# Kernel optimization log

Hardware: AMD Instinct MI355X
Metric: run time of the kernel (lower is better)

## Reference

```python
import jax, jax.numpy as jnp
import numpy as np

HIDDEN = 1024
N_HEADS = 16
HEAD_DIM = HIDDEN // N_HEADS  # 64
SCALE = HEAD_DIM ** -0.5
B, QL, KVL = 2, 2048, 4096


def setup_inputs() -> dict:
    key = jax.random.key(0)
    ks = jax.random.split(key, 7)
    s = 0.02
    return {
        "query_states": jax.random.normal(ks[0], (B, QL, HIDDEN), jnp.float32),
        "key_states": jax.random.normal(ks[1], (B, KVL, HIDDEN), jnp.float32),
        "value_states": jax.random.normal(ks[2], (B, KVL, HIDDEN), jnp.float32),
        # torch nn.Linear weights: shape [out, in], applied as x @ W.T
        "Wq": jax.random.normal(ks[3], (HIDDEN, HIDDEN), jnp.float32) * s,
        "Wk": jax.random.normal(ks[4], (HIDDEN, HIDDEN), jnp.float32) * s,
        "Wv": jax.random.normal(ks[5], (HIDDEN, HIDDEN), jnp.float32) * s,
        "Wo": jax.random.normal(ks[6], (HIDDEN, HIDDEN), jnp.float32) * s,
    }


def reference(query_states, key_states, value_states, Wq, Wk, Wv, Wo):
    b, ql, _ = query_states.shape
    kvl = key_states.shape[1]
    # projections (torch Linear: x @ W.T)
    q = query_states @ Wq.T  # [b, ql, H]
    k = key_states @ Wk.T    # [b, kvl, H]
    v = value_states @ Wv.T  # [b, kvl, H]
    # split heads -> [b, h, s, d]
    q = q.reshape(b, ql, N_HEADS, HEAD_DIM).transpose(0, 2, 1, 3)
    k = k.reshape(b, kvl, N_HEADS, HEAD_DIM).transpose(0, 2, 1, 3)
    v = v.reshape(b, kvl, N_HEADS, HEAD_DIM).transpose(0, 2, 1, 3)
    # scores [b, h, ql, kvl]
    scores = jnp.einsum("bhqd,bhkd->bhqk", q, k) * SCALE
    attn = jax.nn.softmax(scores, axis=-1)
    out = jnp.einsum("bhqk,bhkd->bhqd", attn, v)  # [b, h, ql, d]
    out = out.transpose(0, 2, 1, 3).reshape(b, ql, HIDDEN)
    return out @ Wo.T
```

## Files before the change

kernel.cpp:

```cpp
#include <hip/hip_runtime.h>

#define HID   1024
#define NH    16
#define HD    64
#define QL    2048
#define KVL   4096
#define NB    2
#define QSCALE 0.180336880111120426f

typedef short s8v  __attribute__((ext_vector_type(8)));
typedef short s4v  __attribute__((ext_vector_type(4)));
typedef float f4v  __attribute__((ext_vector_type(4)));

__device__ __forceinline__ unsigned short f2bf(float f) {
  unsigned int u = __builtin_bit_cast(unsigned int, f);
  u += 0x7FFFu + ((u >> 16) & 1u);
  return (unsigned short)(u >> 16);
}

__device__ __forceinline__ float fexp2(float x) {
#if __has_builtin(__builtin_amdgcn_exp2f)
  return __builtin_amdgcn_exp2f(x);
#else
  return exp2f(x);
#endif
}

__global__ __launch_bounds__(256)
void cast_all(const float* __restrict__ q, const float* __restrict__ k,
              const float* __restrict__ v, const float* __restrict__ wq,
              const float* __restrict__ wk, const float* __restrict__ wv,
              const float* __restrict__ wo, unsigned short* __restrict__ dst) {
  size_t c = (size_t)blockIdx.x * 256 + threadIdx.x;
  const float* src; size_t lc; float sc = 1.0f;
  if (c < 524288)       { src = q;  lc = c; }
  else if (c < 1572864) { src = k;  lc = c - 524288; }
  else if (c < 2621440) { src = v;  lc = c - 1572864; }
  else if (c < 2752512) { src = wq; lc = c - 2621440; sc = QSCALE; }
  else if (c < 2883584) { src = wk; lc = c - 2752512; }
  else if (c < 3014656) { src = wv; lc = c - 2883584; }
  else                  { src = wo; lc = c - 3014656; }
  const float4* p = (const float4*)(src + lc * 8);
  float4 a = p[0], b = p[1];
  union { s8v v8; unsigned short h[8]; } u;
  u.h[0] = f2bf(a.x * sc); u.h[1] = f2bf(a.y * sc);
  u.h[2] = f2bf(a.z * sc); u.h[3] = f2bf(a.w * sc);
  u.h[4] = f2bf(b.x * sc); u.h[5] = f2bf(b.y * sc);
  u.h[6] = f2bf(b.z * sc); u.h[7] = f2bf(b.w * sc);
  *(s8v*)(dst + c * 8) = u.v8;
}

typedef const __attribute__((address_space(1))) unsigned int* gas_t;
typedef __attribute__((address_space(3))) unsigned int*       las_t;

__device__ __forceinline__ void gl_lds16(const unsigned short* g, unsigned short* l) {
  __builtin_amdgcn_global_load_lds((gas_t)(const void*)g, (las_t)(void*)l, 16, 0, 0);
}

template <int NJ, bool OUT_BF16>
__device__ __forceinline__ void gemm_body(const unsigned short* __restrict__ A,
                                          const unsigned short* __restrict__ B,
                                          void* __restrict__ Cv, int N, int K,
                                          int bx, int by,
                                          unsigned short* As, unsigned short* Bs) {
  constexpr int TBN = NJ * 32;
  constexpr int WN  = TBN / 2;
  const int tid  = threadIdx.x;
  const int wave = tid >> 6, lane = tid & 63;
  const int wm = wave >> 1, wn = wave & 1;
  const int quad = lane >> 4, l15 = lane & 15;
  const int row0 = by * 128;
  const int col0 = bx * TBN;
  const int srow = lane >> 2;
  const int scol = (lane & 3) * 8;

  f4v acc[4][NJ] = {};

  for (int k0 = 0; k0 < K; k0 += 32) {
    __syncthreads();
#pragma unroll
    for (int cc = 0; cc < 2; cc++) {
      int c = wave + cc * 4;
      gl_lds16(A + (size_t)(row0 + c * 16 + srow) * K + k0 + scol, &As[c * 512]);
    }
    if (NJ == 4) {
#pragma unroll
      for (int cc = 0; cc < 2; cc++) {
        int c = wave + cc * 4;
        gl_lds16(B + (size_t)(col0 + c * 16 + srow) * K + k0 + scol, &Bs[c * 512]);
      }
    } else {
      gl_lds16(B + (size_t)(col0 + wave * 16 + srow) * K + k0 + scol, &Bs[wave * 512]);
    }
    __syncthreads();

    s8v af[4], bf[NJ];
#pragma unroll
    for (int i = 0; i < 4; i++)
      af[i] = *(const s8v*)&As[(wm * 64 + i * 16 + l15) * 32 + quad * 8];
#pragma unroll
    for (int j = 0; j < NJ; j++)
      bf[j] = *(const s8v*)&Bs[(wn * WN + j * 16 + l15) * 32 + quad * 8];
#pragma unroll
    for (int i = 0; i < 4; i++)
#pragma unroll
      for (int j = 0; j < NJ; j++)
        acc[i][j] = __builtin_amdgcn_mfma_f32_16x16x32_bf16(af[i], bf[j],
                                                            acc[i][j], 0, 0, 0);
  }

#pragma unroll
  for (int i = 0; i < 4; i++) {
#pragma unroll
    for (int j = 0; j < NJ; j++) {
      int r = row0 + wm * 64 + i * 16 + quad * 4;
      int c = col0 + wn * WN + j * 16 + l15;
#pragma unroll
      for (int reg = 0; reg < 4; reg++) {
        float v = acc[i][j][reg];
        if constexpr (OUT_BF16)
          ((unsigned short*)Cv)[(size_t)(r + reg) * N + c] = f2bf(v);
        else
          ((float*)Cv)[(size_t)(r + reg) * N + c] = v;
      }
    }
  }
}

__global__ __launch_bounds__(256, 2)
void proj_fused(const unsigned short* __restrict__ qc, const unsigned short* __restrict__ kc,
                const unsigned short* __restrict__ vc, const unsigned short* __restrict__ wqc,
                const unsigned short* __restrict__ wkc, const unsigned short* __restrict__ wvc,
                unsigned short* __restrict__ qp, unsigned short* __restrict__ kp,
                unsigned short* __restrict__ vpt) {
  __shared__ unsigned short As[128 * 32];
  __shared__ unsigned short Bs[128 * 32];
  int bid = blockIdx.x;
  if (bid < 512) {
    gemm_body<2, true>(qc, wqc, qp, HID, HID, bid & 15, bid >> 4, As, Bs);
  } else if (bid < 1536) {
    int l = bid - 512;
    gemm_body<2, true>(kc, wkc, kp, HID, HID, l & 15, l >> 4, As, Bs);
  } else {
    int l = bid - 1536;
    int b = l >> 8, r = l & 255;
    gemm_body<4, true>(wvc, vc + (size_t)b * KVL * HID,
                       vpt + (size_t)b * HID * KVL, KVL, HID, r & 31, r >> 5, As, Bs);
  }
}

__global__ __launch_bounds__(256, 2)
void o_gemm(const unsigned short* __restrict__ ao, const unsigned short* __restrict__ woc,
            float* __restrict__ out) {
  __shared__ unsigned short As[128 * 32];
  __shared__ unsigned short Bs[128 * 32];
  int bid = blockIdx.x;
  gemm_body<2, false>(ao, woc, out, HID, HID, bid & 15, bid >> 4, As, Bs);
}

#define LDSK 40

template <typename T>
__device__ __forceinline__ void stage_tile(unsigned short* dst, const T* src,
                                           int ld, int tid, float sc) {
#pragma unroll
  for (int rep = 0; rep < 2; rep++) {
    int s = rep * 256 + tid;
    int row = s >> 2;
    int cs  = (s & 3) * 8;
    const T* p = src + (size_t)row * ld + cs;
    s8v val;
    if constexpr (sizeof(T) == 4) {
      float4 f0 = *(const float4*)p;
      float4 f1 = *(const float4*)(p + 4);
      union { s8v v; unsigned short h[8]; } u;
      u.h[0] = f2bf(f0.x * sc); u.h[1] = f2bf(f0.y * sc);
      u.h[2] = f2bf(f0.z * sc); u.h[3] = f2bf(f0.w * sc);
      u.h[4] = f2bf(f1.x * sc); u.h[5] = f2bf(f1.y * sc);
      u.h[6] = f2bf(f1.z * sc); u.h[7] = f2bf(f1.w * sc);
      val = u.v;
    } else {
      val = *(const s8v*)p;
    }
    *(s8v*)&dst[row * LDSK + cs] = val;
  }
}

template <typename TA, typename TB, bool OUT_BF16>
__global__ __launch_bounds__(256)
void gemm_conv(const TA* __restrict__ A, const TB* __restrict__ B,
               void* __restrict__ Cv, int M, int N, int K, float bscale,
               long long bz, long long cz) {
  __shared__ unsigned short As[128 * LDSK];
  __shared__ unsigned short Bs[128 * LDSK];
  const TB* Bp = B + (size_t)blockIdx.z * (size_t)bz;
  const int tid  = threadIdx.x;
  const int wave = tid >> 6, lane = tid & 63;
  const int wm = wave >> 1, wn = wave & 1;
  const int quad = lane >> 4, l15 = lane & 15;
  const int row0 = blockIdx.y * 128;
  const int col0 = blockIdx.x * 128;

  f4v acc[4][4] = {};

  for (int k0 = 0; k0 < K; k0 += 32) {
    __syncthreads();
    stage_tile(As, A + (size_t)row0 * K + k0, K, tid, 1.0f);
    stage_tile(Bs, Bp + (size_t)col0 * K + k0, K, tid, bscale);
    __syncthreads();

    s8v af[4], bf[4];
#pragma unroll
    for (int i = 0; i < 4; i++)
      af[i] = *(const s8v*)&As[(wm * 64 + i * 16 + l15) * LDSK + quad * 8];
#pragma unroll
    for (int j = 0; j < 4; j++)
      bf[j] = *(const s8v*)&Bs[(wn * 64 + j * 16 + l15) * LDSK + quad * 8];
#pragma unroll
    for (int i = 0; i < 4; i++)
#pragma unroll
      for (int j = 0; j < 4; j++)
        acc[i][j] = __builtin_amdgcn_mfma_f32_16x16x32_bf16(af[i], bf[j],
                                                            acc[i][j], 0, 0, 0);
  }

  char* Cp = (char*)Cv + (size_t)blockIdx.z * (size_t)cz * (OUT_BF16 ? 2 : 4);
#pragma unroll
  for (int i = 0; i < 4; i++) {
#pragma unroll
    for (int j = 0; j < 4; j++) {
      int r = row0 + wm * 64 + i * 16 + quad * 4;
      int c = col0 + wn * 64 + j * 16 + l15;
#pragma unroll
      for (int reg = 0; reg < 4; reg++) {
        float v = acc[i][j][reg];
        if constexpr (OUT_BF16)
          ((unsigned short*)Cp)[(size_t)(r + reg) * N + c] = f2bf(v);
        else
          ((float*)Cp)[(size_t)(r + reg) * N + c] = v;
      }
    }
  }
}

#define AST 72

__global__ __launch_bounds__(256, 2)
void attn3(const unsigned short* __restrict__ qp,
           const unsigned short* __restrict__ kp,
           const unsigned short* __restrict__ vpt,
           unsigned short* __restrict__ ao) {
  __shared__ unsigned short Ks[64 * AST];
  __shared__ unsigned short Vt[64 * AST];
  __shared__ unsigned short Pt[4][32 * AST];

  const int bid  = blockIdx.x;
  const int qb   = bid & 15;
  const int h    = (bid >> 4) & 15;
  const int b    = bid >> 8;
  const int tid  = threadIdx.x;
  const int wave = tid >> 6, lane = tid & 63;
  const int quad = lane >> 4, l15 = lane & 15;
  const int q0   = qb * 128 + wave * 32;

  int srow[2], scs[2];
#pragma unroll
  for (int rep = 0; rep < 2; rep++) {
    int s = rep * 256 + tid;
    srow[rep] = s >> 3;
    scs[rep]  = (s & 7) * 8;
  }

  s8v qf[2][2];
#pragma unroll
  for (int qt = 0; qt < 2; qt++) {
    const size_t qrow = (size_t)(b * QL + q0 + qt * 16 + l15) * HID + h * HD;
#pragma unroll
    for (int ks = 0; ks < 2; ks++)
      qf[qt][ks] = *(const s8v*)(qp + qrow + ks * 32 + quad * 8);
  }

  float lrun[2] = {0.f, 0.f};
  f4v oacc[2][4] = {};

  const unsigned short* kbase = kp + (size_t)b * KVL * HID + h * HD;
  const unsigned short* vbase = vpt + (size_t)(b * NH + h) * HD * KVL;

  s8v kreg[2], vreg[2];
#pragma unroll
  for (int rep = 0; rep < 2; rep++) {
    kreg[rep] = *(const s8v*)(kbase + (size_t)srow[rep] * HID + scs[rep]);
    vreg[rep] = *(const s8v*)(vbase + (size_t)srow[rep] * KVL + scs[rep]);
  }

  for (int kt = 0; kt < KVL / 64; kt++) {
    __syncthreads();
#pragma unroll
    for (int rep = 0; rep < 2; rep++) {
      *(s8v*)&Ks[srow[rep] * AST + scs[rep]] = kreg[rep];
      *(s8v*)&Vt[srow[rep] * AST + scs[rep]] = vreg[rep];
    }
    if (kt + 1 < KVL / 64) {
      int kv0n = (kt + 1) * 64;
#pragma unroll
      for (int rep = 0; rep < 2; rep++) {
        kreg[rep] = *(const s8v*)(kbase + (size_t)(kv0n + srow[rep]) * HID + scs[rep]);
        vreg[rep] = *(const s8v*)(vbase + (size_t)srow[rep] * KVL + kv0n + scs[rep]);
      }
    }
    __syncthreads();

    f4v sacc[2][4] = {};
#pragma unroll
    for (int nt = 0; nt < 4; nt++) {
      s8v kf0 = *(const s8v*)&Ks[(nt * 16 + l15) * AST + quad * 8];
      s8v kf1 = *(const s8v*)&Ks[(nt * 16 + l15) * AST + 32 + quad * 8];
#pragma unroll
      for (int qt = 0; qt < 2; qt++) {
        sacc[qt][nt] = __builtin_amdgcn_mfma_f32_16x16x32_bf16(kf0, qf[qt][0], sacc[qt][nt], 0, 0, 0);
        sacc[qt][nt] = __builtin_amdgcn_mfma_f32_16x16x32_bf16(kf1, qf[qt][1], sacc[qt][nt], 0, 0, 0);
      }
    }

#pragma unroll
    for (int qt = 0; qt < 2; qt++) {
      float rs = 0.f;
#pragma unroll
      for (int nt = 0; nt < 4; nt++) {
        float p0 = fexp2(sacc[qt][nt][0]);
        float p1 = fexp2(sacc[qt][nt][1]);
        float p2 = fexp2(sacc[qt][nt][2]);
        float p3 = fexp2(sacc[qt][nt][3]);
        rs += (p0 + p1) + (p2 + p3);
        union { s4v v4; unsigned short h[4]; } pk;
        pk.h[0] = f2bf(p0); pk.h[1] = f2bf(p1);
        pk.h[2] = f2bf(p2); pk.h[3] = f2bf(p3);
        *(s4v*)&Pt[wave][(qt * 16 + l15) * AST + nt * 16 + quad * 4] = pk.v4;
      }
      rs += __shfl_xor(rs, 16, 64);
      rs += __shfl_xor(rs, 32, 64);
      lrun[qt] += rs;
    }

#pragma unroll
    for (int ch = 0; ch < 2; ch++) {
      s8v vf[4];
#pragma unroll
      for (int dt = 0; dt < 4; dt++)
        vf[dt] = *(const s8v*)&Vt[(dt * 16 + l15) * AST + ch * 32 + quad * 8];
#pragma unroll
      for (int qt = 0; qt < 2; qt++) {
        s8v pf = *(const s8v*)&Pt[wave][(qt * 16 + l15) * AST + ch * 32 + quad * 8];
#pragma unroll
        for (int dt = 0; dt < 4; dt++)
          oacc[qt][dt] = __builtin_amdgcn_mfma_f32_16x16x32_bf16(pf, vf[dt], oacc[qt][dt], 0, 0, 0);
      }
    }
  }

#pragma unroll
  for (int qt = 0; qt < 2; qt++) {
    float li = 1.0f / lrun[qt];
    float lr[4];
#pragma unroll
    for (int r = 0; r < 4; r++)
      lr[r] = __shfl(li, (lane & 48) + ((lane >> 4) & 3) * 4 + r, 64);
#pragma unroll
    for (int dt = 0; dt < 4; dt++)
#pragma unroll
      for (int r = 0; r < 4; r++) {
        int qq = q0 + qt * 16 + quad * 4 + r;
        int cc = h * HD + dt * 16 + l15;
        ao[(size_t)(b * QL + qq) * HID + cc] = f2bf(oacc[qt][dt][r] * lr[r]);
      }
  }
}

extern "C" void kernel_launch(void* const* d_in, const int* in_sizes, int n_in,
                              void* d_out, int out_size, void* d_ws, size_t ws_size,
                              hipStream_t stream) {
  const float* q  = (const float*)d_in[0];
  const float* k  = (const float*)d_in[1];
  const float* v  = (const float*)d_in[2];
  const float* Wq = (const float*)d_in[3];
  const float* Wk = (const float*)d_in[4];
  const float* Wv = (const float*)d_in[5];
  const float* Wo = (const float*)d_in[6];
  float* out = (float*)d_out;
  char* ws = (char*)d_ws;
  dim3 blk(256);

  const long long MB = 1024 * 1024;
  if (ws_size >= (size_t)88 * MB) {
    unsigned short* qc  = (unsigned short*)(ws);
    unsigned short* kc  = (unsigned short*)(ws + 8 * MB);
    unsigned short* vc  = (unsigned short*)(ws + 24 * MB);
    unsigned short* wqc = (unsigned short*)(ws + 40 * MB);
    unsigned short* wkc = (unsigned short*)(ws + 42 * MB);
    unsigned short* wvc = (unsigned short*)(ws + 44 * MB);
    unsigned short* woc = (unsigned short*)(ws + 46 * MB);
    unsigned short* qp  = (unsigned short*)(ws + 48 * MB);
    unsigned short* kp  = (unsigned short*)(ws + 56 * MB);
    unsigned short* vpt = (unsigned short*)(ws + 72 * MB);
    unsigned short* ao  = (unsigned short*)(ws);

    cast_all<<<12288, blk, 0, stream>>>(q, k, v, Wq, Wk, Wv, Wo, (unsigned short*)ws);
    proj_fused<<<2048, blk, 0, stream>>>(qc, kc, vc, wqc, wkc, wvc, qp, kp, vpt);
    attn3<<<dim3(NB * NH * (QL / 128)), blk, 0, stream>>>(qp, kp, vpt, ao);
    o_gemm<<<512, blk, 0, stream>>>(ao, woc, out);
  } else {
    unsigned short* qp  = (unsigned short*)(ws);
    unsigned short* kp  = (unsigned short*)(ws + 8 * MB);
    unsigned short* vpt = (unsigned short*)(ws + 24 * MB);
    unsigned short* ao  = (unsigned short*)(ws + 40 * MB);

    gemm_conv<float, float, true><<<dim3(8, 32), blk, 0, stream>>>(q, Wq, qp, NB * QL, HID, HID, QSCALE, 0, 0);
    gemm_conv<float, float, true><<<dim3(8, 64), blk, 0, stream>>>(k, Wk, kp, NB * KVL, HID, HID, 1.0f, 0, 0);
    gemm_conv<float, float, true><<<dim3(32, 8, 2), blk, 0, stream>>>(Wv, v, vpt, HID, KVL, HID, 1.0f,
                                                                      (long long)KVL * HID, (long long)HID * KVL);
    attn3<<<dim3(NB * NH * (QL / 128)), blk, 0, stream>>>(qp, kp, vpt, ao);
    gemm_conv<unsigned short, float, false><<<dim3(8, 32), blk, 0, stream>>>(ao, Wo, out, NB * QL, HID, HID, 1.0f, 0, 0);
  }
}
```

Baseline: 320.1 us.

## Enlarge attention query tile and triple-buffer K/V via async LDS loads

Attention blocks now process 256 queries, 64 per wave, and use a three-stage ring of K/V tiles filled with direct global-to-LDS loads and an XOR-swizzled layout instead of register staging with padding. The projection and output GEMMs switch to uniform 128x128 tiles, which halves the block counts. The aim is to raise K/V reuse per load and overlap memory with MFMA work. In exchange, occupancy drops to one block per CU, only 256 attention blocks are launched, and register pressure rises.

```diff
diff --git a/kernel.cpp b/kernel.cpp
--- a/kernel.cpp
+++ b/kernel.cpp
@@ -57,24 +57,22 @@
   __builtin_amdgcn_global_load_lds((gas_t)(const void*)g, (las_t)(void*)l, 16, 0, 0);
 }
 
-template <int NJ, bool OUT_BF16>
+template <bool OUT_BF16>
 __device__ __forceinline__ void gemm_body(const unsigned short* __restrict__ A,
                                           const unsigned short* __restrict__ B,
                                           void* __restrict__ Cv, int N, int K,
                                           int bx, int by,
                                           unsigned short* As, unsigned short* Bs) {
-  constexpr int TBN = NJ * 32;
-  constexpr int WN  = TBN / 2;
   const int tid  = threadIdx.x;
   const int wave = tid >> 6, lane = tid & 63;
   const int wm = wave >> 1, wn = wave & 1;
   const int quad = lane >> 4, l15 = lane & 15;
   const int row0 = by * 128;
-  const int col0 = bx * TBN;
+  const int col0 = bx * 128;
   const int srow = lane >> 2;
   const int scol = (lane & 3) * 8;
 
-  f4v acc[4][NJ] = {};
+  f4v acc[4][4] = {};
 
   for (int k0 = 0; k0 < K; k0 += 32) {
     __syncthreads();
@@ -82,29 +80,21 @@
     for (int cc = 0; cc < 2; cc++) {
       int c = wave + cc * 4;
       gl_lds16(A + (size_t)(row0 + c * 16 + srow) * K + k0 + scol, &As[c * 512]);
-    }
-    if (NJ == 4) {
-#pragma unroll
-      for (int cc = 0; cc < 2; cc++) {
-        int c = wave + cc * 4;
-        gl_lds16(B + (size_t)(col0 + c * 16 + srow) * K + k0 + scol, &Bs[c * 512]);
-      }
-    } else {
-      gl_lds16(B + (size_t)(col0 + wave * 16 + srow) * K + k0 + scol, &Bs[wave * 512]);
+      gl_lds16(B + (size_t)(col0 + c * 16 + srow) * K + k0 + scol, &Bs[c * 512]);
     }
     __syncthreads();
 
-    s8v af[4], bf[NJ];
+    s8v af[4], bf[4];
 #pragma unroll
     for (int i = 0; i < 4; i++)
       af[i] = *(const s8v*)&As[(wm * 64 + i * 16 + l15) * 32 + quad * 8];
 #pragma unroll
-    for (int j = 0; j < NJ; j++)
-      bf[j] = *(const s8v*)&Bs[(wn * WN + j * 16 + l15) * 32 + quad * 8];
+    for (int j = 0; j < 4; j++)
+      bf[j] = *(const s8v*)&Bs[(wn * 64 + j * 16 + l15) * 32 + quad * 8];
 #pragma unroll
     for (int i = 0; i < 4; i++)
 #pragma unroll
-      for (int j = 0; j < NJ; j++)
+      for (int j = 0; j < 4; j++)
         acc[i][j] = __builtin_amdgcn_mfma_f32_16x16x32_bf16(af[i], bf[j],
                                                             acc[i][j], 0, 0, 0);
   }
@@ -112,9 +102,9 @@
 #pragma unroll
   for (int i = 0; i < 4; i++) {
 #pragma unroll
-    for (int j = 0; j < NJ; j++) {
+    for (int j = 0; j < 4; j++) {
       int r = row0 + wm * 64 + i * 16 + quad * 4;
-      int c = col0 + wn * WN + j * 16 + l15;
+      int c = col0 + wn * 64 + j * 16 + l15;
 #pragma unroll
       for (int reg = 0; reg < 4; reg++) {
         float v = acc[i][j][reg];
@@ -136,16 +126,16 @@
   __shared__ unsigned short As[128 * 32];
   __shared__ unsigned short Bs[128 * 32];
   int bid = blockIdx.x;
-  if (bid < 512) {
-    gemm_body<2, true>(qc, wqc, qp, HID, HID, bid & 15, bid >> 4, As, Bs);
-  } else if (bid < 1536) {
-    int l = bid - 512;
-    gemm_body<2, true>(kc, wkc, kp, HID, HID, l & 15, l >> 4, As, Bs);
+  if (bid < 256) {
+    gemm_body<true>(qc, wqc, qp, HID, HID, bid & 7, bid >> 3, As, Bs);
+  } else if (bid < 768) {
+    int l = bid - 256;
+    gemm_body<true>(kc, wkc, kp, HID, HID, l & 7, l >> 3, As, Bs);
   } else {
-    int l = bid - 1536;
+    int l = bid - 768;
     int b = l >> 8, r = l & 255;
-    gemm_body<4, true>(wvc, vc + (size_t)b * KVL * HID,
-                       vpt + (size_t)b * HID * KVL, KVL, HID, r & 31, r >> 5, As, Bs);
+    gemm_body<true>(wvc, vc + (size_t)b * KVL * HID,
+                    vpt + (size_t)b * HID * KVL, KVL, HID, r & 31, r >> 5, As, Bs);
   }
 }
 
@@ -155,7 +145,7 @@
   __shared__ unsigned short As[128 * 32];
   __shared__ unsigned short Bs[128 * 32];
   int bid = blockIdx.x;
-  gemm_body<2, false>(ao, woc, out, HID, HID, bid & 15, bid >> 4, As, Bs);
+  gemm_body<false>(ao, woc, out, HID, HID, bid & 7, bid >> 3, As, Bs);
 }
 
 #define LDSK 40
@@ -245,126 +235,131 @@
 
 #define AST 72
 
-__global__ __launch_bounds__(256, 2)
-void attn3(const unsigned short* __restrict__ qp,
+__global__ __launch_bounds__(256, 1)
+void attn4(const unsigned short* __restrict__ qp,
            const unsigned short* __restrict__ kp,
            const unsigned short* __restrict__ vpt,
            unsigned short* __restrict__ ao) {
-  __shared__ unsigned short Ks[64 * AST];
-  __shared__ unsigned short Vt[64 * AST];
-  __shared__ unsigned short Pt[4][32 * AST];
+  __shared__ unsigned short Ks[3][64 * 64];
+  __shared__ unsigned short Vt[3][64 * 64];
+  __shared__ unsigned short Pt[4][64 * AST];
 
   const int bid  = blockIdx.x;
-  const int qb   = bid & 15;
-  const int h    = (bid >> 4) & 15;
-  const int b    = bid >> 8;
+  const int qb   = bid & 7;
+  const int h    = (bid >> 3) & 15;
+  const int b    = bid >> 7;
   const int tid  = threadIdx.x;
   const int wave = tid >> 6, lane = tid & 63;
   const int quad = lane >> 4, l15 = lane & 15;
-  const int q0   = qb * 128 + wave * 32;
-
-  int srow[2], scs[2];
-#pragma unroll
-  for (int rep = 0; rep < 2; rep++) {
-    int s = rep * 256 + tid;
-    srow[rep] = s >> 3;
-    scs[rep]  = (s & 7) * 8;
-  }
-
-  s8v qf[2][2];
-#pragma unroll
-  for (int qt = 0; qt < 2; qt++) {
-    const size_t qrow = (size_t)(b * QL + q0 + qt * 16 + l15) * HID + h * HD;
-#pragma unroll
-    for (int ks = 0; ks < 2; ks++)
-      qf[qt][ks] = *(const s8v*)(qp + qrow + ks * 32 + quad * 8);
-  }
-
-  float lrun[2] = {0.f, 0.f};
-  f4v oacc[2][4] = {};
+  const int q0   = qb * 256 + wave * 64;
 
   const unsigned short* kbase = kp + (size_t)b * KVL * HID + h * HD;
   const unsigned short* vbase = vpt + (size_t)(b * NH + h) * HD * KVL;
 
-  s8v kreg[2], vreg[2];
-#pragma unroll
-  for (int rep = 0; rep < 2; rep++) {
-    kreg[rep] = *(const s8v*)(kbase + (size_t)srow[rep] * HID + scs[rep]);
-    vreg[rep] = *(const s8v*)(vbase + (size_t)srow[rep] * KVL + scs[rep]);
-  }
-
-  for (int kt = 0; kt < KVL / 64; kt++) {
-    __syncthreads();
-#pragma unroll
-    for (int rep = 0; rep < 2; rep++) {
-      *(s8v*)&Ks[srow[rep] * AST + scs[rep]] = kreg[rep];
-      *(s8v*)&Vt[srow[rep] * AST + scs[rep]] = vreg[rep];
-    }
-    if (kt + 1 < KVL / 64) {
-      int kv0n = (kt + 1) * 64;
-#pragma unroll
-      for (int rep = 0; rep < 2; rep++) {
-        kreg[rep] = *(const s8v*)(kbase + (size_t)(kv0n + srow[rep]) * HID + scs[rep]);
-        vreg[rep] = *(const s8v*)(vbase + (size_t)srow[rep] * KVL + kv0n + scs[rep]);
-      }
-    }
-    __syncthreads();
-
-    f4v sacc[2][4] = {};
+  int prow[2], pcol[2], pbase[2];
+#pragma unroll
+  for (int i = 0; i < 2; i++) {
+    int p = (i * 4 + wave) * 64 + lane;
+    prow[i]  = p >> 3;
+    pcol[i]  = ((p & 7) ^ (prow[i] & 7)) * 8;
+    pbase[i] = (i * 4 + wave) * 512;
+  }
+
+  s8v qf[4][2];
+#pragma unroll
+  for (int nt = 0; nt < 4; nt++) {
+    const size_t qrow = (size_t)(b * QL + q0 + nt * 16 + l15) * HID + h * HD;
+#pragma unroll
+    for (int ks = 0; ks < 2; ks++)
+      qf[nt][ks] = *(const s8v*)(qp + qrow + ks * 32 + quad * 8);
+  }
+
+  float lrun[4] = {0.f, 0.f, 0.f, 0.f};
+  f4v oacc[4][4] = {};
+
+#define STAGE_KV(KT, BI)                                                        \
+  {                                                                             \
+    const unsigned short* kb = kbase + (size_t)((KT) * 64) * HID;               \
+    const unsigned short* vb = vbase + (KT) * 64;                               \
+    _Pragma("unroll")                                                           \
+    for (int i = 0; i < 2; i++) {                                               \
+      gl_lds16(kb + (size_t)prow[i] * HID + pcol[i], &Ks[BI][pbase[i]]);        \
+      gl_lds16(vb + (size_t)prow[i] * KVL + pcol[i], &Vt[BI][pbase[i]]);        \
+    }                                                                           \
+  }
+
+  constexpr int NT = KVL / 64;
+  STAGE_KV(0, 0);
+  STAGE_KV(1, 1);
+  __syncthreads();
+
+  for (int kt = 0; kt < NT; kt++) {
+    const int cur = kt % 3;
+    if (kt + 2 < NT) STAGE_KV(kt + 2, (kt + 2) % 3);
+
+    f4v sacc[4][4] = {};
+#pragma unroll
+    for (int ks = 0; ks < 2; ks++)
+#pragma unroll
+      for (int mt = 0; mt < 4; mt++) {
+        int row = mt * 16 + l15;
+        int xc  = ((ks * 4 + quad) ^ (row & 7)) * 8;
+        s8v kf = *(const s8v*)&Ks[cur][row * 64 + xc];
+#pragma unroll
+        for (int nt = 0; nt < 4; nt++)
+          sacc[mt][nt] = __builtin_amdgcn_mfma_f32_16x16x32_bf16(kf, qf[nt][ks],
+                                                                 sacc[mt][nt], 0, 0, 0);
+      }
+
 #pragma unroll
     for (int nt = 0; nt < 4; nt++) {
-      s8v kf0 = *(const s8v*)&Ks[(nt * 16 + l15) * AST + quad * 8];
-      s8v kf1 = *(const s8v*)&Ks[(nt * 16 + l15) * AST + 32 + quad * 8];
-#pragma unroll
-      for (int qt = 0; qt < 2; qt++) {
-        sacc[qt][nt] = __builtin_amdgcn_mfma_f32_16x16x32_bf16(kf0, qf[qt][0], sacc[qt][nt], 0, 0, 0);
-        sacc[qt][nt] = __builtin_amdgcn_mfma_f32_16x16x32_bf16(kf1, qf[qt][1], sacc[qt][nt], 0, 0, 0);
-      }
-    }
-
-#pragma unroll
-    for (int qt = 0; qt < 2; qt++) {
       float rs = 0.f;
 #pragma unroll
-      for (int nt = 0; nt < 4; nt++) {
-        float p0 = fexp2(sacc[qt][nt][0]);
-        float p1 = fexp2(sacc[qt][nt][1]);
-        float p2 = fexp2(sacc[qt][nt][2]);
-        float p3 = fexp2(sacc[qt][nt][3]);
+      for (int mt = 0; mt < 4; mt++) {
+        float p0 = fexp2(sacc[mt][nt][0]);
+        float p1 = fexp2(sacc[mt][nt][1]);
+        float p2 = fexp2(sacc[mt][nt][2]);
+        float p3 = fexp2(sacc[mt][nt][3]);
         rs += (p0 + p1) + (p2 + p3);
-        union { s4v v4; unsigned short h[4]; } pk;
-        pk.h[0] = f2bf(p0); pk.h[1] = f2bf(p1);
-        pk.h[2] = f2bf(p2); pk.h[3] = f2bf(p3);
-        *(s4v*)&Pt[wave][(qt * 16 + l15) * AST + nt * 16 + quad * 4] = pk.v4;
+        union { s4v v4; unsigned short hh[4]; } pk;
+        pk.hh[0] = f2bf(p0); pk.hh[1] = f2bf(p1);
+        pk.hh[2] = f2bf(p2); pk.hh[3] = f2bf(p3);
+        *(s4v*)&Pt[wave][(nt * 16 + l15) * AST + mt * 16 + quad * 4] = pk.v4;
       }
       rs += __shfl_xor(rs, 16, 64);
       rs += __shfl_xor(rs, 32, 64);
-      lrun[qt] += rs;
+      lrun[nt] += rs;
     }
 
 #pragma unroll
     for (int ch = 0; ch < 2; ch++) {
       s8v vf[4];
 #pragma unroll
-      for (int dt = 0; dt < 4; dt++)
-        vf[dt] = *(const s8v*)&Vt[(dt * 16 + l15) * AST + ch * 32 + quad * 8];
-#pragma unroll
-      for (int qt = 0; qt < 2; qt++) {
+      for (int dt = 0; dt < 4; dt++) {
+        int row = dt * 16 + l15;
+        int xc  = ((ch * 4 + quad) ^ (row & 7)) * 8;
+        vf[dt] = *(const s8v*)&Vt[cur][row * 64 + xc];
+      }
+#pragma unroll
+      for (int qt = 0; qt < 4; qt++) {
         s8v pf = *(const s8v*)&Pt[wave][(qt * 16 + l15) * AST + ch * 32 + quad * 8];
 #pragma unroll
         for (int dt = 0; dt < 4; dt++)
-          oacc[qt][dt] = __builtin_amdgcn_mfma_f32_16x16x32_bf16(pf, vf[dt], oacc[qt][dt], 0, 0, 0);
-      }
-    }
-  }
-
-#pragma unroll
-  for (int qt = 0; qt < 2; qt++) {
+          oacc[qt][dt] = __builtin_amdgcn_mfma_f32_16x16x32_bf16(pf, vf[dt],
+                                                                 oacc[qt][dt], 0, 0, 0);
+      }
+    }
+
+    __syncthreads();
+  }
+
+#pragma unroll
+  for (int qt = 0; qt < 4; qt++) {
     float li = 1.0f / lrun[qt];
     float lr[4];
 #pragma unroll
     for (int r = 0; r < 4; r++)
-      lr[r] = __shfl(li, (lane & 48) + ((lane >> 4) & 3) * 4 + r, 64);
+      lr[r] = __shfl(li, (lane & 48) + quad * 4 + r, 64);
 #pragma unroll
     for (int dt = 0; dt < 4; dt++)
 #pragma unroll
@@ -374,6 +369,7 @@
         ao[(size_t)(b * QL + qq) * HID + cc] = f2bf(oacc[qt][dt][r] * lr[r]);
       }
   }
+#undef STAGE_KV
 }
 
 extern "C" void kernel_launch(void* const* d_in, const int* in_sizes, int n_in,
@@ -405,9 +401,9 @@
     unsigned short* ao  = (unsigned short*)(ws);
 
     cast_all<<<12288, blk, 0, stream>>>(q, k, v, Wq, Wk, Wv, Wo, (unsigned short*)ws);
-    proj_fused<<<2048, blk, 0, stream>>>(qc, kc, vc, wqc, wkc, wvc, qp, kp, vpt);
-    attn3<<<dim3(NB * NH * (QL / 128)), blk, 0, stream>>>(qp, kp, vpt, ao);
-    o_gemm<<<512, blk, 0, stream>>>(ao, woc, out);
+    proj_fused<<<1280, blk, 0, stream>>>(qc, kc, vc, wqc, wkc, wvc, qp, kp, vpt);
+    attn4<<<256, blk, 0, stream>>>(qp, kp, vpt, ao);
+    o_gemm<<<256, blk, 0, stream>>>(ao, woc, out);
   } else {
     unsigned short* qp  = (unsigned short*)(ws);
     unsigned short* kp  = (unsigned short*)(ws + 8 * MB);
@@ -418,7 +414,7 @@
     gemm_conv<float, float, true><<<dim3(8, 64), blk, 0, stream>>>(k, Wk, kp, NB * KVL, HID, HID, 1.0f, 0, 0);
     gemm_conv<float, float, true><<<dim3(32, 8, 2), blk, 0, stream>>>(Wv, v, vpt, HID, KVL, HID, 1.0f,
                                                                       (long long)KVL * HID, (long long)HID * KVL);
-    attn3<<<dim3(NB * NH * (QL / 128)), blk, 0, stream>>>(qp, kp, vpt, ao);
+    attn4<<<256, blk, 0, stream>>>(qp, kp, vpt, ao);
     gemm_conv<unsigned short, float, false><<<dim3(8, 32), blk, 0, stream>>>(ao, Wo, out, NB * QL, HID, HID, 1.0f, 0, 0);
   }
 }
```

Result: slower. 344.8 us (+7.7%).
